# Kernel tuning notes

Hardware: AMD Instinct MI355X
Metric: run time of the kernel (lower is better)

Reference implementation:

```python
import jax, jax.numpy as jnp
import numpy as np

B, T, D, H, FF_MULT, WINDOW = 4, 2048, 256, 8, 4, 64
HD = D // H
FF = FF_MULT * D
EPS = 1e-5


def _layer_norm(x, g, b):
    m = jnp.mean(x, axis=-1, keepdims=True)
    v = jnp.mean(jnp.square(x - m), axis=-1, keepdims=True)
    return (x - m) / jnp.sqrt(v + EPS) * g + b


def setup_inputs() -> dict:
    key = jax.random.key(0)
    ks = jax.random.split(key, 6)
    scale = 0.02
    return {
        "x": jax.random.normal(ks[0], (B, T, D), jnp.float32),
        "ln1_g": jnp.ones((D,), jnp.float32),
        "ln1_b": jnp.zeros((D,), jnp.float32),
        "in_proj_w": jax.random.normal(ks[1], (D, 3 * D), jnp.float32) * scale,
        "in_proj_b": jnp.zeros((3 * D,), jnp.float32),
        "out_w": jax.random.normal(ks[2], (D, D), jnp.float32) * scale,
        "out_b": jnp.zeros((D,), jnp.float32),
        "ln2_g": jnp.ones((D,), jnp.float32),
        "ln2_b": jnp.zeros((D,), jnp.float32),
        "w1": jax.random.normal(ks[3], (D, FF), jnp.float32) * scale,
        "b1": jnp.zeros((FF,), jnp.float32),
        "w2": jax.random.normal(ks[4], (FF, D), jnp.float32) * scale,
        "b2": jnp.zeros((D,), jnp.float32),
        "window": WINDOW,
    }


def reference(x, ln1_g, ln1_b, in_proj_w, in_proj_b, out_w, out_b,
              ln2_g, ln2_b, w1, b1, w2, b2, window):
    Bv, Tv, Dv = x.shape
    xn = _layer_norm(x, ln1_g, ln1_b)                      # norm1(x) used as q,k,v
    qkv = xn @ in_proj_w + in_proj_b                       # [B,T,3D]
    q, k, v = jnp.split(qkv, 3, axis=-1)

    def to_heads(t):
        return t.reshape(Bv, Tv, H, HD).transpose(0, 2, 1, 3)  # [B,H,T,HD]

    q, k, v = to_heads(q), to_heads(k), to_heads(v)
    scores = jnp.einsum('bhqd,bhkd->bhqk', q, k) / jnp.sqrt(jnp.float32(HD))
    i = jnp.arange(Tv)[:, None]
    j = jnp.arange(Tv)[None, :]
    band = jnp.abs(j - i) <= window                        # True = allowed
    scores = jnp.where(band, scores, -jnp.inf)
    attn = jax.nn.softmax(scores, axis=-1)
    o = jnp.einsum('bhqk,bhkd->bhqd', attn, v)
    o = o.transpose(0, 2, 1, 3).reshape(Bv, Tv, Dv)
    h_out = o @ out_w + out_b                              # attn output
    y = x + h_out
    ff = _layer_norm(y, ln2_g, ln2_b)
    ff = jax.nn.gelu(ff @ w1 + b1, approximate=False) @ w2 + b2
    return x + ff                                          # note: residual from x, not y
```

## Files before the change

kernel.cpp:

```cpp
#include <hip/hip_runtime.h>
#include <math.h>

#define T_SEQ 2048

typedef float  fx4 __attribute__((ext_vector_type(4)));
typedef short  sx4 __attribute__((ext_vector_type(4)));
typedef short  sx8 __attribute__((ext_vector_type(8)));
typedef unsigned short u16;

static __device__ __forceinline__ u16 f2b(float f) {
  unsigned u = __builtin_bit_cast(unsigned, f);
  u += 0x7fffu + ((u >> 16) & 1u);
  return (u16)(u >> 16);
}

static __device__ __forceinline__ fx4 mfma16(sx4 a, sx4 b, fx4 c) {
  return __builtin_amdgcn_mfma_f32_16x16x16bf16_1k(a, b, c, 0, 0, 0);
}
static __device__ __forceinline__ fx4 mfma32(sx8 a, sx8 b, fx4 c) {
  return __builtin_amdgcn_mfma_f32_16x16x32_bf16(a, b, c, 0, 0, 0);
}

static __device__ __forceinline__ void gload16(const void* g, void* l) {
  __builtin_amdgcn_global_load_lds(
      (const __attribute__((address_space(1))) unsigned*)g,
      (__attribute__((address_space(3))) unsigned*)l, 16, 0, 0);
}

__global__ __launch_bounds__(256) void prep_k(
    const float* __restrict__ x, const float* __restrict__ g1,
    const float* __restrict__ b1, u16* __restrict__ xn,
    const float* __restrict__ ipw, const float* __restrict__ outw,
    const float* __restrict__ w1, const float* __restrict__ w2,
    u16* __restrict__ ipwT, u16* __restrict__ outwT,
    u16* __restrict__ w1T, u16* __restrict__ w2T) {
  const int bid = blockIdx.x;
  if (bid < 2048) {
    const int row = bid * 4 + (threadIdx.x >> 6);
    const int l = threadIdx.x & 63;
    fx4 v = *(const fx4*)&x[(size_t)row * 256 + l * 4];
    float s = v.x + v.y + v.z + v.w;
    float q = v.x * v.x + v.y * v.y + v.z * v.z + v.w * v.w;
#pragma unroll
    for (int off = 1; off < 64; off <<= 1) {
      s += __shfl_xor(s, off);
      q += __shfl_xor(q, off);
    }
    const float mean = s * (1.0f / 256.0f);
    const float var = q * (1.0f / 256.0f) - mean * mean;
    const float rstd = rsqrtf(var + 1e-5f);
    fx4 gv = *(const fx4*)&g1[l * 4];
    fx4 bv = *(const fx4*)&b1[l * 4];
    sx4 o;
    o[0] = (short)f2b((v.x - mean) * rstd * gv.x + bv.x);
    o[1] = (short)f2b((v.y - mean) * rstd * gv.y + bv.y);
    o[2] = (short)f2b((v.z - mean) * rstd * gv.z + bv.z);
    o[3] = (short)f2b((v.w - mean) * rstd * gv.w + bv.w);
    *(sx4*)&xn[(size_t)row * 256 + l * 4] = o;
    return;
  }
  const int tb = bid - 2048;
  const float* in; u16* out; int K, N, loc;
  if (tb < 192)      { in = ipw;  out = ipwT;  K = 256;  N = 768;  loc = tb; }
  else if (tb < 256) { in = outw; out = outwT; K = 256;  N = 256;  loc = tb - 192; }
  else if (tb < 512) { in = w1;   out = w1T;   K = 256;  N = 1024; loc = tb - 256; }
  else               { in = w2;   out = w2T;   K = 1024; N = 256;  loc = tb - 512; }
  const int ntx = N >> 5;
  const int by = (loc / ntx) << 5;
  const int bx = (loc % ntx) << 5;
  __shared__ float t[32][33];
  const int c = threadIdx.x & 31, r0 = threadIdx.x >> 5;
#pragma unroll
  for (int i = 0; i < 4; ++i)
    t[r0 + i * 8][c] = in[(size_t)(by + r0 + i * 8) * N + bx + c];
  __syncthreads();
#pragma unroll
  for (int i = 0; i < 4; ++i) {
    const int r = r0 + i * 8;
    out[(size_t)(bx + r) * K + by + c] = f2b(t[c][r]);
  }
}

template <int BM, int BN, int KD, int ND, int OP, int NGRP>
__global__ __launch_bounds__(256) void gemm3_k(const u16* __restrict__ A,
                                               const u16* __restrict__ Wt,
                                               const float* __restrict__ bias,
                                               const float* __restrict__ resid,
                                               void* __restrict__ outp) {
  constexpr int BK = 64;
  constexpr int WM = BM / 2, WN = BN / 2;
  constexpr int FM = WM / 16, FN = WN / 16;
  constexpr int NT = KD / BK;
  __shared__ u16 As[2][BM][BK];
  __shared__ u16 Bs[2][BN][BK];
  const int tid = threadIdx.x;
  const int id = blockIdx.x;
  const int bm = ((id & 7) + 8 * ((id >> 3) / NGRP)) * BM;
  const int bn = ((id >> 3) % NGRP) * BN;
  const int l = tid & 63, wid = tid >> 6;
  const int wm = wid >> 1, wn = wid & 1;
  const int lq = l & 15, lg = l >> 4;

  auto stage = [&](int buf, int k0) {
#pragma unroll
    for (int i = 0; i < (BM * BK) / 2048; ++i) {
      const int row = (tid >> 3) + 32 * i;
      const int c = (tid & 7) ^ (row & 7);
      gload16(&A[(size_t)(bm + row) * KD + k0 + c * 8], &As[buf][row][(tid & 7) * 8]);
    }
#pragma unroll
    for (int i = 0; i < (BN * BK) / 2048; ++i) {
      const int row = (tid >> 3) + 32 * i;
      const int c = (tid & 7) ^ (row & 7);
      gload16(&Wt[(size_t)(bn + row) * KD + k0 + c * 8], &Bs[buf][row][(tid & 7) * 8]);
    }
  };

  fx4 acc[FM][FN] = {};
  stage(0, 0);
  int cur = 0;
  for (int t = 0; t < NT; ++t) {
    __syncthreads();
    if (t + 1 < NT) stage(cur ^ 1, (t + 1) * BK);
#pragma unroll
    for (int kk = 0; kk < BK; kk += 32) {
      sx8 aF[FM], bF[FN];
#pragma unroll
      for (int m = 0; m < FM; ++m) {
        const int row = wm * WM + m * 16 + lq;
        const int c = ((kk >> 3) + lg) ^ (row & 7);
        aF[m] = *(const sx8*)&As[cur][row][c * 8];
      }
#pragma unroll
      for (int n = 0; n < FN; ++n) {
        const int row = wn * WN + n * 16 + lq;
        const int c = ((kk >> 3) + lg) ^ (row & 7);
        bF[n] = *(const sx8*)&Bs[cur][row][c * 8];
      }
#pragma unroll
      for (int m = 0; m < FM; ++m)
#pragma unroll
        for (int n = 0; n < FN; ++n) acc[m][n] = mfma32(aF[m], bF[n], acc[m][n]);
    }
    cur ^= 1;
  }
#pragma unroll
  for (int m = 0; m < FM; ++m) {
#pragma unroll
    for (int n = 0; n < FN; ++n) {
      const int col = bn + wn * WN + n * 16 + lq;
      const float bv = bias[col];
#pragma unroll
      for (int r = 0; r < 4; ++r) {
        const int row = bm + wm * WM + m * 16 + lg * 4 + r;
        float v = acc[m][n][r] + bv;
        if (OP == 1) {
          v += resid[(size_t)row * ND + col];
          ((float*)outp)[(size_t)row * ND + col] = v;
        } else if (OP == 0) {
          ((u16*)outp)[(size_t)row * ND + col] = f2b(v);
        } else {
          const float ge = 0.5f * v * (1.0f + erff(v * 0.70710678118654752f));
          ((u16*)outp)[(size_t)row * ND + col] = f2b(ge);
        }
      }
    }
  }
}

__global__ __launch_bounds__(256) void gemmln_k(const u16* __restrict__ A,
                                                const u16* __restrict__ Wt,
                                                const float* __restrict__ bias,
                                                const float* __restrict__ x,
                                                const float* __restrict__ g,
                                                const float* __restrict__ bv2,
                                                u16* __restrict__ yn) {
  __shared__ u16 As[32][32];
  __shared__ u16 Bs[256][32];
  __shared__ float red[32][2][2];
  const int tid = threadIdx.x;
  const int bm = blockIdx.x * 32;
  const int l = tid & 63, wid = tid >> 6;
  const int wm = wid >> 1, wn = wid & 1;
  const int lq = l & 15, lg = l >> 4;
  const int sr = tid >> 2, sc = (tid & 3) << 3;
  fx4 acc[8] = {};
  for (int k0 = 0; k0 < 256; k0 += 32) {
    if (tid < 128) gload16(&A[(size_t)(bm + (tid >> 2)) * 256 + k0 + ((tid & 3) << 3)],
                           &As[tid >> 2][(tid & 3) << 3]);
#pragma unroll
    for (int i = 0; i < 4; ++i)
      gload16(&Wt[(size_t)(sr + i * 64) * 256 + k0 + sc], &Bs[sr + i * 64][sc]);
    __syncthreads();
    const sx8 aF = *(const sx8*)&As[wm * 16 + lq][8 * lg];
#pragma unroll
    for (int n = 0; n < 8; ++n) {
      const sx8 bF = *(const sx8*)&Bs[wn * 128 + n * 16 + lq][8 * lg];
      acc[n] = mfma32(aF, bF, acc[n]);
    }
    __syncthreads();
  }
  float vv[8][4];
  float s[4] = {}, q[4] = {};
#pragma unroll
  for (int n = 0; n < 8; ++n) {
    const int col = wn * 128 + n * 16 + lq;
    const float bb = bias[col];
#pragma unroll
    for (int r = 0; r < 4; ++r) {
      const int row = bm + wm * 16 + lg * 4 + r;
      const float v = acc[n][r] + bb + x[(size_t)row * 256 + col];
      vv[n][r] = v;
      s[r] += v;
      q[r] += v * v;
    }
  }
#pragma unroll
  for (int off = 1; off < 16; off <<= 1) {
#pragma unroll
    for (int r = 0; r < 4; ++r) {
      s[r] += __shfl_xor(s[r], off);
      q[r] += __shfl_xor(q[r], off);
    }
  }
  if (lq == 0) {
#pragma unroll
    for (int r = 0; r < 4; ++r) {
      red[wm * 16 + lg * 4 + r][wn][0] = s[r];
      red[wm * 16 + lg * 4 + r][wn][1] = q[r];
    }
  }
  __syncthreads();
#pragma unroll
  for (int r = 0; r < 4; ++r) {
    const int rr = wm * 16 + lg * 4 + r;
    const float st = red[rr][0][0] + red[rr][1][0];
    const float qt = red[rr][0][1] + red[rr][1][1];
    const float mean = st * (1.0f / 256.0f);
    const float var = qt * (1.0f / 256.0f) - mean * mean;
    const float rs = rsqrtf(var + 1e-5f);
    const int row = bm + rr;
#pragma unroll
    for (int n = 0; n < 8; ++n) {
      const int col = wn * 128 + n * 16 + lq;
      yn[(size_t)row * 256 + col] = f2b((vv[n][r] - mean) * rs * g[col] + bv2[col]);
    }
  }
}

__global__ __launch_bounds__(512) void attn_k(const u16* __restrict__ qkv,
                                              u16* __restrict__ o) {
  __shared__ u16 Qs[128][32];
  __shared__ u16 Ks[256][32];
  __shared__ u16 Vs[32][264];
  const int blk = blockIdx.x;
  const int tile = blk & 15;
  const int bh = blk >> 4;
  const int h = bh & 7;
  const int b = bh >> 3;
  const int q0 = tile << 7;
  const int kstart = max(0, q0 - 64);
  const int kend = min(T_SEQ, q0 + 192);
  const int nk = kend - kstart;
  const int tid = threadIdx.x;
  const float scale = 0.17677669529663687f;

  {
    const int r = tid >> 2, c8 = (tid & 3) << 3;
    gload16(&qkv[(size_t)(b * T_SEQ + q0 + r) * 768 + h * 32 + c8], &Qs[r][c8]);
  }
  for (int r0 = 0; r0 < nk; r0 += 128) {
    const int r = r0 + (tid >> 2);
    if (r < nk) {
      const int c8 = (tid & 3) << 3;
      gload16(&qkv[(size_t)(b * T_SEQ + kstart + r) * 768 + 256 + h * 32 + c8], &Ks[r][c8]);
    }
  }
  for (int e = tid * 4; e < nk * 32; e += 2048) {
    const int r = e >> 5, c = e & 31;
    sx4 v = *(const sx4*)&qkv[(size_t)(b * T_SEQ + kstart + r) * 768 + 512 + h * 32 + c];
    Vs[c + 0][r] = v[0];
    Vs[c + 1][r] = v[1];
    Vs[c + 2][r] = v[2];
    Vs[c + 3][r] = v[3];
  }
  __syncthreads();

  const int w = tid >> 6, l = tid & 63;
  const int lq = l & 15, lg = l >> 4;
  const int qw0 = q0 + w * 16;
  const int iq = qw0 + lq;
  const sx8 qB = *(const sx8*)&Qs[w * 16 + lq][8 * lg];
  float lsum = 0.0f;
  fx4 acc0 = {0.f, 0.f, 0.f, 0.f}, acc1 = {0.f, 0.f, 0.f, 0.f};
  const int rt0 = max(0, qw0 - 64 - kstart) >> 4;
  const int rt1 = (min(kend, qw0 + 80) - kstart) >> 4;
  for (int rt = rt0; rt < rt1; ++rt) {
    const int kb = kstart + (rt << 4);
    const sx8 kA = *(const sx8*)&Ks[(rt << 4) + lq][8 * lg];
    fx4 zero = {0.f, 0.f, 0.f, 0.f};
    fx4 sc = mfma32(kA, qB, zero);
    sx4 pB;
#pragma unroll
    for (int r = 0; r < 4; ++r) {
      const int dd = kb + 4 * lg + r - iq;
      const float sv = (dd >= -64 && dd <= 64) ? fminf(sc[r] * scale, 30.0f) : -100.0f;
      const float p = __expf(sv);
      lsum += p;
      pB[r] = (short)f2b(p);
    }
    const sx4 vA0 = *(const sx4*)&Vs[lq][(rt << 4) + 4 * lg];
    const sx4 vA1 = *(const sx4*)&Vs[16 + lq][(rt << 4) + 4 * lg];
    acc0 = mfma16(vA0, pB, acc0);
    acc1 = mfma16(vA1, pB, acc1);
  }
  lsum += __shfl_xor(lsum, 16);
  lsum += __shfl_xor(lsum, 32);
  const float rl = 1.0f / lsum;
  const size_t obase = (size_t)(b * T_SEQ + qw0 + lq) * 256 + h * 32;
  sx4 ov;
  ov[0] = (short)f2b(acc0[0] * rl);
  ov[1] = (short)f2b(acc0[1] * rl);
  ov[2] = (short)f2b(acc0[2] * rl);
  ov[3] = (short)f2b(acc0[3] * rl);
  *(sx4*)&o[obase + 4 * lg] = ov;
  ov[0] = (short)f2b(acc1[0] * rl);
  ov[1] = (short)f2b(acc1[1] * rl);
  ov[2] = (short)f2b(acc1[2] * rl);
  ov[3] = (short)f2b(acc1[3] * rl);
  *(sx4*)&o[obase + 16 + 4 * lg] = ov;
}

extern "C" void kernel_launch(void* const* d_in, const int* in_sizes, int n_in,
                              void* d_out, int out_size, void* d_ws, size_t ws_size,
                              hipStream_t stream) {
  const float* x    = (const float*)d_in[0];
  const float* ln1g = (const float*)d_in[1];
  const float* ln1b = (const float*)d_in[2];
  const float* ipw  = (const float*)d_in[3];
  const float* ipb  = (const float*)d_in[4];
  const float* outw = (const float*)d_in[5];
  const float* outb = (const float*)d_in[6];
  const float* ln2g = (const float*)d_in[7];
  const float* ln2b = (const float*)d_in[8];
  const float* w1   = (const float*)d_in[9];
  const float* b1   = (const float*)d_in[10];
  const float* w2   = (const float*)d_in[11];
  const float* b2   = (const float*)d_in[12];

  char* ws = (char*)d_ws;
  u16*   xn   = (u16*)(ws);
  u16*   qkvb = (u16*)(ws + (4ull << 20));
  u16*   o    = (u16*)(ws + (16ull << 20));
  u16*   yn   = (u16*)(ws + (20ull << 20));
  u16*   hh   = (u16*)(ws + (24ull << 20));
  u16*   ipwT = (u16*)(ws + (40ull << 20));
  u16*   outwT= (u16*)(ws + (40ull << 20) + (512ull << 10));
  u16*   w1T  = (u16*)(ws + (41ull << 20));
  u16*   w2T  = (u16*)(ws + (41ull << 20) + (512ull << 10));

  prep_k<<<2816, 256, 0, stream>>>(x, ln1g, ln1b, xn, ipw, outw, w1, w2,
                                   ipwT, outwT, w1T, w2T);
  gemm3_k<64, 128, 256, 768, 0, 6><<<768, 256, 0, stream>>>(xn, ipwT, ipb, nullptr, qkvb);
  attn_k<<<512, 512, 0, stream>>>(qkvb, o);
  gemmln_k<<<256, 256, 0, stream>>>(o, outwT, outb, x, ln2g, ln2b, yn);
  gemm3_k<64, 128, 256, 1024, 2, 8><<<1024, 256, 0, stream>>>(yn, w1T, b1, nullptr, hh);
  gemm3_k<64, 128, 1024, 256, 1, 2><<<256, 256, 0, stream>>>(hh, w2T, b2, x, (float*)d_out);
}
```

Baseline: 69.25 us.

## Stage epilogue outputs through shared memory for coalesced vector stores

The GEMM, GEMM+LayerNorm and attention epilogues now write results into a shared-memory tile first, then issue wide 16-byte coalesced global stores in place of scattered 2- or 4-byte per-lane writes. For the residual GEMM, the residual read is also vectorised. This is meant to cut the number of global store transactions and uncoalesced traffic. The cost is extra barriers and LDS round trips, plus reuse of the staging buffers, which requires the added synchronisation.

```diff
diff --git a/kernel.cpp b/kernel.cpp
--- a/kernel.cpp
+++ b/kernel.cpp
@@ -91,8 +91,9 @@
   constexpr int WM = BM / 2, WN = BN / 2;
   constexpr int FM = WM / 16, FN = WN / 16;
   constexpr int NT = KD / BK;
-  __shared__ u16 As[2][BM][BK];
-  __shared__ u16 Bs[2][BN][BK];
+  __shared__ __align__(16) char smem[(2 * BM + 2 * BN) * BK * 2];
+  auto As = (u16(*)[BM][BK])smem;
+  auto Bs = (u16(*)[BN][BK])(smem + 2 * BM * BK * 2);
   const int tid = threadIdx.x;
   const int id = blockIdx.x;
   const int bm = ((id & 7) + 8 * ((id >> 3) / NGRP)) * BM;
@@ -144,26 +145,53 @@
     }
     cur ^= 1;
   }
-#pragma unroll
-  for (int m = 0; m < FM; ++m) {
-#pragma unroll
-    for (int n = 0; n < FN; ++n) {
-      const int col = bn + wn * WN + n * 16 + lq;
-      const float bv = bias[col];
-#pragma unroll
-      for (int r = 0; r < 4; ++r) {
-        const int row = bm + wm * WM + m * 16 + lg * 4 + r;
-        float v = acc[m][n][r] + bv;
-        if (OP == 1) {
-          v += resid[(size_t)row * ND + col];
-          ((float*)outp)[(size_t)row * ND + col] = v;
-        } else if (OP == 0) {
-          ((u16*)outp)[(size_t)row * ND + col] = f2b(v);
-        } else {
-          const float ge = 0.5f * v * (1.0f + erff(v * 0.70710678118654752f));
-          ((u16*)outp)[(size_t)row * ND + col] = f2b(ge);
+
+  __syncthreads();
+  if (OP == 1) {
+    auto C = (float(*)[BN + 8])smem;
+#pragma unroll
+    for (int m = 0; m < FM; ++m)
+#pragma unroll
+      for (int n = 0; n < FN; ++n) {
+        const int col = wn * WN + n * 16 + lq;
+        const float bv = bias[bn + col];
+#pragma unroll
+        for (int r = 0; r < 4; ++r)
+          C[wm * WM + m * 16 + lg * 4 + r][col] = acc[m][n][r] + bv;
+      }
+    __syncthreads();
+    constexpr int CH = (BM * BN / 4) / 256;
+#pragma unroll
+    for (int i = 0; i < CH; ++i) {
+      const int t = tid + i * 256;
+      const int row = t / (BN / 4), c = t % (BN / 4);
+      fx4 v = *(const fx4*)&C[row][c * 4];
+      const fx4 rr = *(const fx4*)&resid[(size_t)(bm + row) * ND + bn + c * 4];
+      v += rr;
+      *(fx4*)&((float*)outp)[(size_t)(bm + row) * ND + bn + c * 4] = v;
+    }
+  } else {
+    auto C = (u16(*)[BN + 8])smem;
+#pragma unroll
+    for (int m = 0; m < FM; ++m)
+#pragma unroll
+      for (int n = 0; n < FN; ++n) {
+        const int col = wn * WN + n * 16 + lq;
+        const float bv = bias[bn + col];
+#pragma unroll
+        for (int r = 0; r < 4; ++r) {
+          float v = acc[m][n][r] + bv;
+          if (OP == 2) v = 0.5f * v * (1.0f + erff(v * 0.70710678118654752f));
+          C[wm * WM + m * 16 + lg * 4 + r][col] = f2b(v);
         }
       }
+    __syncthreads();
+    constexpr int CH = (BM * BN / 8) / 256;
+#pragma unroll
+    for (int i = 0; i < CH; ++i) {
+      const int t = tid + i * 256;
+      const int row = t / (BN / 8), c = t % (BN / 8);
+      *(sx8*)&((u16*)outp)[(size_t)(bm + row) * ND + bn + c * 8] = *(const sx8*)&C[row][c * 8];
     }
   }
 }
@@ -175,9 +203,11 @@
                                                 const float* __restrict__ g,
                                                 const float* __restrict__ bv2,
                                                 u16* __restrict__ yn) {
-  __shared__ u16 As[32][32];
-  __shared__ u16 Bs[256][32];
-  __shared__ float red[32][2][2];
+  __shared__ __align__(16) char smem[18944];
+  auto As = (u16(*)[32])smem;
+  auto Bs = (u16(*)[32])(smem + 2048);
+  auto red = (float(*)[2][2])(smem + 18432);
+  auto Ys = (u16(*)[264])smem;
   const int tid = threadIdx.x;
   const int bm = blockIdx.x * 32;
   const int l = tid & 63, wid = tid >> 6;
@@ -231,20 +261,31 @@
     }
   }
   __syncthreads();
+  float mean4[4], rs4[4];
 #pragma unroll
   for (int r = 0; r < 4; ++r) {
     const int rr = wm * 16 + lg * 4 + r;
     const float st = red[rr][0][0] + red[rr][1][0];
     const float qt = red[rr][0][1] + red[rr][1][1];
-    const float mean = st * (1.0f / 256.0f);
-    const float var = qt * (1.0f / 256.0f) - mean * mean;
-    const float rs = rsqrtf(var + 1e-5f);
-    const int row = bm + rr;
-#pragma unroll
-    for (int n = 0; n < 8; ++n) {
-      const int col = wn * 128 + n * 16 + lq;
-      yn[(size_t)row * 256 + col] = f2b((vv[n][r] - mean) * rs * g[col] + bv2[col]);
-    }
+    mean4[r] = st * (1.0f / 256.0f);
+    const float var = qt * (1.0f / 256.0f) - mean4[r] * mean4[r];
+    rs4[r] = rsqrtf(var + 1e-5f);
+  }
+  __syncthreads();
+#pragma unroll
+  for (int n = 0; n < 8; ++n) {
+    const int col = wn * 128 + n * 16 + lq;
+    const float gc = g[col], bc = bv2[col];
+#pragma unroll
+    for (int r = 0; r < 4; ++r)
+      Ys[wm * 16 + lg * 4 + r][col] = f2b((vv[n][r] - mean4[r]) * rs4[r] * gc + bc);
+  }
+  __syncthreads();
+#pragma unroll
+  for (int i = 0; i < 4; ++i) {
+    const int t = tid + i * 256;
+    const int row = t >> 5, c = t & 31;
+    *(sx8*)&yn[(size_t)(bm + row) * 256 + c * 8] = *(const sx8*)&Ys[row][c * 8];
   }
 }
 
@@ -317,18 +358,20 @@
   lsum += __shfl_xor(lsum, 16);
   lsum += __shfl_xor(lsum, 32);
   const float rl = 1.0f / lsum;
-  const size_t obase = (size_t)(b * T_SEQ + qw0 + lq) * 256 + h * 32;
-  sx4 ov;
-  ov[0] = (short)f2b(acc0[0] * rl);
-  ov[1] = (short)f2b(acc0[1] * rl);
-  ov[2] = (short)f2b(acc0[2] * rl);
-  ov[3] = (short)f2b(acc0[3] * rl);
-  *(sx4*)&o[obase + 4 * lg] = ov;
-  ov[0] = (short)f2b(acc1[0] * rl);
-  ov[1] = (short)f2b(acc1[1] * rl);
-  ov[2] = (short)f2b(acc1[2] * rl);
-  ov[3] = (short)f2b(acc1[3] * rl);
-  *(sx4*)&o[obase + 16 + 4 * lg] = ov;
+
+  __syncthreads();
+  auto Os = (u16(*)[32])Qs;
+#pragma unroll
+  for (int r = 0; r < 4; ++r) {
+    Os[w * 16 + lq][4 * lg + r] = f2b(acc0[r] * rl);
+    Os[w * 16 + lq][16 + 4 * lg + r] = f2b(acc1[r] * rl);
+  }
+  __syncthreads();
+  {
+    const int row = tid >> 2, c = tid & 3;
+    *(sx8*)&o[(size_t)(b * T_SEQ + q0 + row) * 256 + h * 32 + c * 8] =
+        *(const sx8*)&Os[row][c * 8];
+  }
 }
 
 extern "C" void kernel_launch(void* const* d_in, const int* in_sizes, int n_in,
```

After: 64.00 us. 1.08x faster.
